# Performance work log

Hardware: AMD Instinct MI355X
Metric: run time of the kernel (lower is better)

The kernel has to match this reference:

```python
import jax, jax.numpy as jnp
import numpy as np

DIM = 1024
B = 8192
DT_REF_BASE = 1.0


def _cayley(raw_re, raw_im):
    # A = skew-Hermitian-ish combo per original code
    A = (raw_re - raw_re.T) * 0.5 + 1j * ((raw_im + raw_im.T) * 0.5)
    I = jnp.eye(A.shape[0], dtype=A.dtype)
    return jnp.linalg.solve(I - A, I + A)


def setup_inputs() -> dict:
    key = jax.random.key(0)
    ks = jax.random.split(key, 16)
    d = DIM
    g = d // 2  # n_groups = 2, equal group sizes
    return {
        "h_prev": jax.random.normal(ks[0], (B, d), jnp.float32),
        "x_input": jax.random.normal(ks[1], (B, d), jnp.float32),
        "dt": jax.random.uniform(ks[2], (B,), jnp.float32),
        "u_raw_re": jax.random.normal(ks[3], (d, d), jnp.float32) * 0.01,
        "u_raw_im": jax.random.normal(ks[4], (d, d), jnp.float32) * 0.01,
        "v_raw_re": jax.random.normal(ks[5], (d, d), jnp.float32) * 0.01,
        "v_raw_im": jax.random.normal(ks[6], (d, d), jnp.float32) * 0.01,
        "log_sigma": jnp.zeros((d,), jnp.float32),
        "ld": jax.random.normal(ks[7], (d,), jnp.float32) * 0.5 - 2.0,
        "lf": jnp.concatenate([
            2.0 * jax.random.normal(ks[8], (g,), jnp.float32),
            0.1 * jax.random.normal(ks[9], (g,), jnp.float32),
        ]),
        "dt_scaler": jnp.concatenate([0.1 * jnp.ones((g,), jnp.float32),
                                      10.0 * jnp.ones((g,), jnp.float32)]),
        "src_re": jax.random.normal(ks[10], (d,), jnp.float32) * 0.01,
        "src_im": jax.random.normal(ks[11], (d,), jnp.float32) * 0.01,
        "law_re": jax.random.normal(ks[12], (d,), jnp.float32) * 0.01,
        "law_im": jax.random.normal(ks[13], (d,), jnp.float32) * 0.01,
        "sel_w": jax.random.normal(ks[14], (2 * d, 2 * d), jnp.float32) * 0.01,
        "sel_b": jax.random.normal(ks[15], (2 * d,), jnp.float32) * 0.01,
    }


def reference(h_prev, x_input, dt, u_raw_re, u_raw_im, v_raw_re, v_raw_im,
              log_sigma, ld, lf, dt_scaler, src_re, src_im, law_re, law_im,
              sel_w, sel_b):
    # --- Cayley basis (shared between encode/decode) ---
    U = _cayley(u_raw_re, u_raw_im)                       # [D, D] complex
    V = _cayley(v_raw_re, v_raw_im)
    s = jnp.exp(log_sigma).astype(U.dtype)
    s_inv = jnp.exp(-log_sigma).astype(U.dtype)
    M_inv = (V * s_inv[None, :]) @ U.conj().T             # V @ diag(1/s) @ U^H
    M = (U * s[None, :]) @ V.conj().T                     # U @ diag(s) @ V^H

    encode = lambda x: x.astype(M_inv.dtype) @ M_inv.T
    h_tilde = encode(h_prev)[:, None, :]                  # [B, 1, D]
    x_tilde = encode(x_input)[:, None, :]                 # [B, 1, D]
    x_state = x_tilde[:, 0, :]                            # [B, D]

    # --- selective Lambda ---
    lam_static = (-jnp.exp(ld) + 1j * lf) + (law_re + 1j * law_im)  # [D]
    x_cat = jnp.concatenate([x_state.real, x_state.imag], axis=-1)  # [B, 2D]
    delta = x_cat @ sel_w.T + sel_b                                  # [B, 2D]
    d_re, d_im = jnp.split(delta, 2, axis=-1)
    Lam = lam_static[None, :] + (d_re + 1j * d_im)                   # [B, D]

    # --- transition operators ---
    dt_ref_eff = DT_REF_BASE * dt_scaler                  # [D]
    dt_n = dt[:, None] / dt_ref_eff                       # [B, D]
    Z = Lam * dt_n.astype(Lam.dtype)
    mask = jnp.abs(Z) < 1e-4
    safe_Z = jnp.where(mask, jnp.ones_like(Z), Z)
    phi1 = jnp.where(mask, 1.0 + 0.5 * Z + Z * Z / 6.0,
                     (jnp.exp(Z) - 1.0) / safe_Z)
    op_decay = jnp.exp(Z)                                 # [B, D]
    op_forcing = phi1 * (dt_n * dt_ref_eff).astype(Z.dtype)

    bias = src_re + 1j * src_im                           # [D]
    h_next = h_tilde * op_decay[:, None, :] + (x_tilde + bias) * op_forcing[:, None, :]
    # eval mode / noise term omitted (deterministic reference)
    return h_next @ M.T                                   # [B, 1, D] complex64
```

## Files before the change

### kernel.cpp

```cpp
#include <hip/hip_runtime.h>
#include <hip/hip_bf16.h>

#define Dd 1024
#define Bb 8192

typedef unsigned short u16;
typedef __attribute__((ext_vector_type(8))) short short8;
typedef __attribute__((ext_vector_type(4))) float f32x4;
typedef __attribute__((ext_vector_type(4))) float float4v;

static constexpr size_t DD  = (size_t)Dd * Dd;
static constexpr size_t BD  = (size_t)Bb * Dd;
static constexpr size_t MBy = 1ull << 20;

__device__ __forceinline__ float bf2f(u16 v) {
  union { unsigned u; float f; } c; c.u = ((unsigned)v) << 16; return c.f;
}
__device__ __forceinline__ u16 f2bf(float f) {
  union { float f; unsigned u; } c; c.f = f;
  return (u16)((c.u + 0x7fffu + ((c.u >> 16) & 1u)) >> 16);
}

union U64 { u16 u[4]; unsigned long long v; };

struct ZP { const u16* Ah; const u16* Al; const u16* Bh; const u16* Bl; void* C; void* C2; float alpha; float beta; };
struct GArgs { ZP z[8]; int K, lda, ldb; long ldc; int cstride; };

template<int OUT>
__device__ __forceinline__ void c_store(const ZP& p, long cidx, float acc) {
  float v = acc * p.alpha;
  if constexpr (OUT == 1) {
    ((u16*)p.C)[cidx] = f2bf(v);
  } else if constexpr (OUT == 2) {
    u16 h = f2bf(v);
    ((u16*)p.C)[cidx] = h;
    ((u16*)p.C2)[cidx] = f2bf(v - bf2f(h));
  } else {
    float* C = (float*)p.C;
    if (p.beta != 0.0f) v += p.beta * C[cidx];
    C[cidx] = v;
  }
}

template<int MODE, int OUT, int BN>
__global__ __launch_bounds__(256) void gemm_nt(GArgs a) {
  constexpr bool X2 = (MODE != 0);
  constexpr int BK  = X2 ? 32 : 64;
  constexpr int NJ  = BN / 32;
  constexpr int BUFS = 8192 + BN * 64;
  constexpr int BHOFF = 4096;
  constexpr int ALOFF = 4096 + BN * 32;
  constexpr int BLOFF = 8192 + BN * 32;
  __shared__ __align__(16) u16 smem[2 * BUFS];
  const ZP p = a.z[blockIdx.z];
  const int tid  = threadIdx.x;
  const int lane = tid & 63, wv = tid >> 6;

  int bx = blockIdx.x, by = blockIdx.y;
  {
    const int gx = gridDim.x;
    const int nwg = gx * gridDim.y;
    if ((nwg & 7) == 0 && nwg >= 16) {
      const int flat = by * gx + bx;
      const int ch = nwg >> 3;
      const int nf = (flat & 7) * ch + (flat >> 3);
      bx = nf % gx; by = nf / gx;
    }
  }

  const long brow = (long)by * 128, bcol = (long)bx * BN;
  const int wm = (wv & 1) * 64, wn = (wv >> 1) * (BN / 2);
  const int srow = wv * 8 + (lane >> 3);
  const int sgc64 = ((lane & 7) ^ (lane >> 3)) * 8;
  const int sgc32 = ((tid & 3) ^ ((tid >> 3) & 3)) * 8;

  f32x4 acc[4][NJ];
#pragma unroll
  for (int i = 0; i < 4; ++i)
#pragma unroll
    for (int j = 0; j < NJ; ++j) { f32x4 zv = {0.f, 0.f, 0.f, 0.f}; acc[i][j] = zv; }

  auto STAGE = [&](int kt, int buf) {
    u16* base = smem + buf * BUFS;
    if constexpr (!X2) {
      u16* As = base;
      u16* Bs = base + 8192;
#pragma unroll
      for (int i = 0; i < 4; ++i) {
        const int rr = i * 32 + srow;
        const int lb = (i * 32 + wv * 8) * 64;
        const u16* ga = p.Ah + (brow + rr) * (long)a.lda + kt + sgc64;
        __builtin_amdgcn_global_load_lds((const __attribute__((address_space(1))) void*)ga,
                                         (__attribute__((address_space(3))) void*)(As + lb), 16, 0, 0);
      }
#pragma unroll
      for (int i = 0; i < BN / 32; ++i) {
        const int rr = i * 32 + srow;
        const int lb = (i * 32 + wv * 8) * 64;
        const u16* gb = p.Bh + (bcol + rr) * (long)a.ldb + kt + sgc64;
        __builtin_amdgcn_global_load_lds((const __attribute__((address_space(1))) void*)gb,
                                         (__attribute__((address_space(3))) void*)(Bs + lb), 16, 0, 0);
      }
    } else {
#pragma unroll
      for (int pass = 0; pass < 2; ++pass) {
        const int row = pass * 64 + (tid >> 2);
        const int lb = pass * 2048 + tid * 8;
        const u16* ga = p.Ah + (brow + row) * (long)a.lda + kt + sgc32;
        const u16* ga2 = p.Al + (brow + row) * (long)a.lda + kt + sgc32;
        __builtin_amdgcn_global_load_lds((const __attribute__((address_space(1))) void*)ga,
                                         (__attribute__((address_space(3))) void*)(base + lb), 16, 0, 0);
        __builtin_amdgcn_global_load_lds((const __attribute__((address_space(1))) void*)ga2,
                                         (__attribute__((address_space(3))) void*)(base + ALOFF + lb), 16, 0, 0);
      }
#pragma unroll
      for (int pass = 0; pass < BN / 64; ++pass) {
        const int row = pass * 64 + (tid >> 2);
        const int lb = pass * 2048 + tid * 8;
        const u16* gb = p.Bh + (bcol + row) * (long)a.ldb + kt + sgc32;
        const u16* gb2 = p.Bl + (bcol + row) * (long)a.ldb + kt + sgc32;
        __builtin_amdgcn_global_load_lds((const __attribute__((address_space(1))) void*)gb,
                                         (__attribute__((address_space(3))) void*)(base + BHOFF + lb), 16, 0, 0);
        __builtin_amdgcn_global_load_lds((const __attribute__((address_space(1))) void*)gb2,
                                         (__attribute__((address_space(3))) void*)(base + BLOFF + lb), 16, 0, 0);
      }
    }
  };

  auto COMPUTE = [&](int buf) {
    u16* base = smem + buf * BUFS;
    if constexpr (!X2) {
      u16* As = base;
      u16* Bs = base + 8192;
#pragma unroll
      for (int kk = 0; kk < 64; kk += 32) {
        const int jf = (kk >> 3) + (lane >> 4);
        const int cs = ((jf ^ (lane & 7)) << 3);
        short8 af[4], bfv[NJ];
#pragma unroll
        for (int i = 0; i < 4; ++i)
          af[i] = *(const short8*)(As + (wm + i * 16 + (lane & 15)) * 64 + cs);
#pragma unroll
        for (int j = 0; j < NJ; ++j)
          bfv[j] = *(const short8*)(Bs + (wn + j * 16 + (lane & 15)) * 64 + cs);
#pragma unroll
        for (int i = 0; i < 4; ++i)
#pragma unroll
          for (int j = 0; j < NJ; ++j)
            acc[i][j] = __builtin_amdgcn_mfma_f32_16x16x32_bf16(af[i], bfv[j], acc[i][j], 0, 0, 0);
      }
    } else {
      const int jf = lane >> 4;
      const int cs = ((jf ^ ((lane >> 1) & 3)) << 3);
      short8 af[4], al[4], bfv[NJ], bl[NJ];
#pragma unroll
      for (int i = 0; i < 4; ++i) {
        const int ra = (wm + i * 16 + (lane & 15)) * 32 + cs;
        af[i] = *(const short8*)(base + ra);
        al[i] = *(const short8*)(base + ALOFF + ra);
      }
#pragma unroll
      for (int j = 0; j < NJ; ++j) {
        const int rb = (wn + j * 16 + (lane & 15)) * 32 + cs;
        bfv[j] = *(const short8*)(base + BHOFF + rb);
        bl[j]  = *(const short8*)(base + BLOFF + rb);
      }
#pragma unroll
      for (int i = 0; i < 4; ++i)
#pragma unroll
        for (int j = 0; j < NJ; ++j) {
          acc[i][j] = __builtin_amdgcn_mfma_f32_16x16x32_bf16(af[i], bfv[j], acc[i][j], 0, 0, 0);
          acc[i][j] = __builtin_amdgcn_mfma_f32_16x16x32_bf16(al[i], bfv[j], acc[i][j], 0, 0, 0);
          acc[i][j] = __builtin_amdgcn_mfma_f32_16x16x32_bf16(af[i], bl[j], acc[i][j], 0, 0, 0);
        }
    }
  };

  const int nkt = a.K / BK;
  STAGE(0, 0);
  __syncthreads();
  int cur = 0;
  for (int t = 0; t < nkt - 1; ++t) {
    STAGE((t + 1) * BK, cur ^ 1);
    COMPUTE(cur);
    __syncthreads();
    cur ^= 1;
  }
  COMPUTE(cur);

  const long crow = brow + wm + ((lane >> 4) * 4);
  const long ccol = bcol + wn + (lane & 15);
#pragma unroll
  for (int i = 0; i < 4; ++i)
#pragma unroll
    for (int j = 0; j < NJ; ++j)
#pragma unroll
      for (int r = 0; r < 4; ++r) {
        const long cidx = (crow + i * 16 + r) * a.ldc + (ccol + j * 16) * (long)a.cstride;
        c_store<OUT>(p, cidx, acc[i][j][r]);
      }
}

template<int OUT>
__global__ __launch_bounds__(512, 1) void gemm_nt256(GArgs a) {
  constexpr int BUFS = 32768;
  __shared__ __align__(16) u16 smem[2 * BUFS];
  const ZP p = a.z[blockIdx.z];
  const int tid  = threadIdx.x;
  const int lane = tid & 63, wv = tid >> 6;
  const int wr = wv >> 2, wc = wv & 3;

  int bx = blockIdx.x, by = blockIdx.y;
  {
    const int gx = gridDim.x;
    const int nwg = gx * gridDim.y;
    if ((nwg & 7) == 0 && nwg >= 16) {
      const int flat = by * gx + bx;
      const int ch = nwg >> 3;
      const int nf = (flat & 7) * ch + (flat >> 3);
      bx = nf % gx; by = nf / gx;
    }
  }

  const long brow = (long)by * 256, bcol = (long)bx * 256;
  const int sgc = ((tid & 7) ^ ((tid >> 3) & 7)) * 8;

  f32x4 acc[8][4];
#pragma unroll
  for (int i = 0; i < 8; ++i)
#pragma unroll
    for (int j = 0; j < 4; ++j) { f32x4 zv = {0.f, 0.f, 0.f, 0.f}; acc[i][j] = zv; }

  auto STAGE = [&](int kt, int buf) {
    u16* As = smem + buf * BUFS;
    u16* Bs = As + 16384;
#pragma unroll
    for (int i = 0; i < 4; ++i) {
      const int rr = i * 64 + (tid >> 3);
      const int lb = i * 4096 + tid * 8;
      const u16* ga = p.Ah + (brow + rr) * (long)a.lda + kt + sgc;
      const u16* gb = p.Bh + (bcol + rr) * (long)a.ldb + kt + sgc;
      __builtin_amdgcn_global_load_lds((const __attribute__((address_space(1))) void*)ga,
                                       (__attribute__((address_space(3))) void*)(As + lb), 16, 0, 0);
      __builtin_amdgcn_global_load_lds((const __attribute__((address_space(1))) void*)gb,
                                       (__attribute__((address_space(3))) void*)(Bs + lb), 16, 0, 0);
    }
  };

  auto COMPUTE = [&](int buf) {
    u16* As = smem + buf * BUFS;
    u16* Bs = As + 16384;
#pragma unroll
    for (int kk = 0; kk < 64; kk += 32) {
      const int jf = (kk >> 3) + (lane >> 4);
      const int cs = ((jf ^ (lane & 7)) << 3);
      short8 af[8], bfv[4];
#pragma unroll
      for (int i = 0; i < 8; ++i)
        af[i] = *(const short8*)(As + (wr * 128 + i * 16 + (lane & 15)) * 64 + cs);
#pragma unroll
      for (int j = 0; j < 4; ++j)
        bfv[j] = *(const short8*)(Bs + (wc * 64 + j * 16 + (lane & 15)) * 64 + cs);
#pragma unroll
      for (int i = 0; i < 8; ++i)
#pragma unroll
        for (int j = 0; j < 4; ++j)
          acc[i][j] = __builtin_amdgcn_mfma_f32_16x16x32_bf16(af[i], bfv[j], acc[i][j], 0, 0, 0);
    }
  };

  const int nkt = a.K >> 6;
  STAGE(0, 0);
  __syncthreads();
  int cur = 0;
  for (int t = 0; t < nkt - 1; ++t) {
    STAGE((t + 1) * 64, cur ^ 1);
    COMPUTE(cur);
    __syncthreads();
    cur ^= 1;
  }
  COMPUTE(cur);

  const long crow = brow + wr * 128 + ((lane >> 4) * 4);
  const long ccol = bcol + wc * 64 + (lane & 15);
#pragma unroll
  for (int i = 0; i < 8; ++i)
#pragma unroll
    for (int j = 0; j < 4; ++j)
#pragma unroll
      for (int r = 0; r < 4; ++r) {
        const long cidx = (crow + i * 16 + r) * a.ldc + (ccol + j * 16) * (long)a.cstride;
        c_store<OUT>(p, cidx, acc[i][j][r]);
      }
}

#define TLOAD(ldsbuf, srcp) do { \
  _Pragma("unroll") \
  for (int i_ = 0; i_ < 4; ++i_) { \
    int row_ = ty + i_ * 16; \
    float4v v_ = *(const float4v*)((srcp) + (size_t)row_ * Dd + tx * 4); \
    ldsbuf[row_][tx * 4 + 0] = v_[0]; ldsbuf[row_][tx * 4 + 1] = v_[1]; \
    ldsbuf[row_][tx * 4 + 2] = v_[2]; ldsbuf[row_][tx * 4 + 3] = v_[3]; \
  } } while (0)

__global__ void k_buildA(const float* ur, const float* ui, const float* vr, const float* vi,
                         float* Af32, u16* Ahi, u16* Alo, u16* AsumH, u16* AsumL) {
  __shared__ float ldsA[64][65], ldsB[64][65];
  const int y = blockIdx.z;
  const int tx = threadIdx.x & 15, ty = threadIdx.x >> 4;
  const int R0 = blockIdx.y * 64, C0 = blockIdx.x * 64;
  const float* re = y ? vr : ur; const float* im = y ? vi : ui;
  TLOAD(ldsA, re + (size_t)C0 * Dd + R0);
  TLOAD(ldsB, im + (size_t)C0 * Dd + R0);
  __syncthreads();
#pragma unroll
  for (int i = 0; i < 4; ++i) {
    const int r = R0 + ty + i * 16;
    const size_t base = (size_t)r * Dd + C0 + tx * 4;
    float4v vre = *(const float4v*)(re + base);
    float4v vim = *(const float4v*)(im + base);
    float4v oar, oai;
    U64 ph, pl, pih, pil, sh, sl;
#pragma unroll
    for (int j = 0; j < 4; ++j) {
      float are = 0.5f * (vre[j] - ldsA[tx * 4 + j][ty + i * 16]);
      float aim = 0.5f * (vim[j] + ldsB[tx * 4 + j][ty + i * 16]);
      oar[j] = are; oai[j] = aim;
      u16 h = f2bf(are); ph.u[j] = h; pl.u[j] = f2bf(are - bf2f(h));
      h = f2bf(aim); pih.u[j] = h; pil.u[j] = f2bf(aim - bf2f(h));
      float s = are + aim; h = f2bf(s); sh.u[j] = h; sl.u[j] = f2bf(s - bf2f(h));
    }
    const size_t pr = (size_t)y * 2 * DD + base, pi = pr + DD;
    *(float4v*)(Af32 + pr) = oar; *(float4v*)(Af32 + pi) = oai;
    *(unsigned long long*)(Ahi + pr) = ph.v; *(unsigned long long*)(Alo + pr) = pl.v;
    *(unsigned long long*)(Ahi + pi) = pih.v; *(unsigned long long*)(Alo + pi) = pil.v;
    const size_t ps = (size_t)y * DD + base;
    *(unsigned long long*)(AsumH + ps) = sh.v; *(unsigned long long*)(AsumL + ps) = sl.v;
  }
}

__global__ void k_sq(const float* T, float* A2u, float* A2v, u16* A2T, u16* A2Tsum) {
  __shared__ float ldsA[64][65], ldsB[64][65];
  const int y = blockIdx.z;
  const int tx = threadIdx.x & 15, ty = threadIdx.x >> 4;
  const int R0 = blockIdx.y * 64, C0 = blockIdx.x * 64;
  const float* t0p = T + (size_t)y * 3 * DD;
  const float* t2p = t0p + 2 * DD;
  TLOAD(ldsA, t2p + (size_t)C0 * Dd + R0);
  __syncthreads();
  float* A2 = y ? A2v : A2u;
  float xr[4][4], xi[4][4];
#pragma unroll
  for (int i = 0; i < 4; ++i) {
    const size_t base = (size_t)(R0 + ty + i * 16) * Dd + C0 + tx * 4;
    float4v v0 = *(const float4v*)(t0p + base);
    float4v v1 = *(const float4v*)(t0p + DD + base);
    float4v v2 = *(const float4v*)(t2p + base);
    float4v oar, oai;
#pragma unroll
    for (int j = 0; j < 4; ++j) {
      float a2re = -v0[j] - v1[j];
      float a2im = v2[j] - ldsA[tx * 4 + j][ty + i * 16];
      xr[i][j] = a2re; xi[i][j] = a2im;
      oar[j] = a2re; oai[j] = a2im;
    }
    *(float4v*)(A2 + base) = oar;
    *(float4v*)(A2 + DD + base) = oai;
  }
  __syncthreads();
#pragma unroll
  for (int i = 0; i < 4; ++i)
#pragma unroll
    for (int j = 0; j < 4; ++j) {
      ldsA[ty + i * 16][tx * 4 + j] = xr[i][j];
      ldsB[ty + i * 16][tx * 4 + j] = xi[i][j];
    }
  __syncthreads();
#pragma unroll
  for (int i = 0; i < 4; ++i) {
    const int cc = C0 + ty + i * 16;
    const size_t tb = (size_t)cc * Dd + R0 + tx * 4;
    U64 ph, pih, sh;
#pragma unroll
    for (int j = 0; j < 4; ++j) {
      float a2re = ldsA[tx * 4 + j][ty + i * 16];
      float a2im = ldsB[tx * 4 + j][ty + i * 16];
      ph.u[j] = f2bf(a2re); pih.u[j] = f2bf(a2im);
      sh.u[j] = f2bf(a2re + a2im);
    }
    const size_t qr = (size_t)y * 2 * DD + tb;
    *(unsigned long long*)(A2T + qr) = ph.v;
    *(unsigned long long*)(A2T + qr + DD) = pih.v;
    *(unsigned long long*)(A2Tsum + (size_t)y * DD + tb) = sh.v;
  }
}

__global__ void k_x0n(const float* Af32, const float* A2u, const float* A2v, const float* T,
                      float* Xf32, u16* Xhi, u16* XThi, u16* XsumH, u16* XTsumH) {
  __shared__ float ldsA[64][65], ldsB[64][65];
  const int y = blockIdx.z;
  const int tx = threadIdx.x & 15, ty = threadIdx.x >> 4;
  const int R0 = blockIdx.y * 64, C0 = blockIdx.x * 64;
  const float* t0p = T + (size_t)y * 3 * DD;
  const float* A2 = y ? A2v : A2u;
  float xr[4][4], xi[4][4];
#pragma unroll
  for (int i = 0; i < 4; ++i) {
    const int r = R0 + ty + i * 16;
    const size_t base = (size_t)r * Dd + C0 + tx * 4;
    float4v v0 = *(const float4v*)(t0p + base);
    float4v v1 = *(const float4v*)(t0p + DD + base);
    float4v v2 = *(const float4v*)(t0p + 2 * DD + base);
    const size_t pr = (size_t)y * 2 * DD + base, pi = pr + DD;
    float4v ar = *(const float4v*)(Af32 + pr);
    float4v ai = *(const float4v*)(Af32 + pi);
    float4v a2r = *(const float4v*)(A2 + base);
    float4v a2i = *(const float4v*)(A2 + DD + base);
    float4v oxr, oxi;
    U64 ph, pih, sh;
#pragma unroll
    for (int j = 0; j < 4; ++j) {
      const int c = C0 + tx * 4 + j;
      float xre = ar[j] + a2r[j] + (v0[j] - v1[j]) + (r == c ? 1.0f : 0.0f);
      float xim = ai[j] + a2i[j] + (v2[j] - v0[j] - v1[j]);
      xr[i][j] = xre; xi[i][j] = xim;
      oxr[j] = xre; oxi[j] = xim;
      ph.u[j] = f2bf(xre); pih.u[j] = f2bf(xim);
      sh.u[j] = f2bf(xre + xim);
    }
    *(float4v*)(Xf32 + pr) = oxr; *(float4v*)(Xf32 + pi) = oxi;
    *(unsigned long long*)(Xhi + pr) = ph.v; *(unsigned long long*)(Xhi + pi) = pih.v;
    *(unsigned long long*)(XsumH + (size_t)y * DD + base) = sh.v;
  }
  __syncthreads();
#pragma unroll
  for (int i = 0; i < 4; ++i)
#pragma unroll
    for (int j = 0; j < 4; ++j) {
      ldsA[ty + i * 16][tx * 4 + j] = xr[i][j];
      ldsB[ty + i * 16][tx * 4 + j] = xi[i][j];
    }
  __syncthreads();
#pragma unroll
  for (int i = 0; i < 4; ++i) {
    const int cc = C0 + ty + i * 16;
    const size_t tb = (size_t)cc * Dd + R0 + tx * 4;
    U64 ph, pih, sh;
#pragma unroll
    for (int j = 0; j < 4; ++j) {
      float xre = ldsA[tx * 4 + j][ty + i * 16];
      float xim = ldsB[tx * 4 + j][ty + i * 16];
      ph.u[j] = f2bf(xre); pih.u[j] = f2bf(xim);
      sh.u[j] = f2bf(xre + xim);
    }
    const size_t qr = (size_t)y * 2 * DD + tb;
    *(unsigned long long*)(XThi + qr) = ph.v;
    *(unsigned long long*)(XThi + qr + DD) = pih.v;
    *(unsigned long long*)(XTsumH + (size_t)y * DD + tb) = sh.v;
  }
}

__global__ void k_wt(const float* Xf32, const float* T, u16* WThi, u16* WTsumH, float idc) {
  __shared__ float lds[64][65];
  const int y = blockIdx.z;
  const int tx = threadIdx.x & 15, ty = threadIdx.x >> 4;
  const int N0 = blockIdx.y * 64, K0 = blockIdx.x * 64;
  const float* t1p = T + (size_t)y * 3 * DD;
  const float* xrp = Xf32 + (size_t)y * 2 * DD;
  float wre[4][4], wim[4][4];
#pragma unroll
  for (int i = 0; i < 4; ++i)
#pragma unroll
    for (int j = 0; j < 4; ++j) {
      wre[i][j] = ((N0 + ty + i * 16) == (K0 + tx * 4 + j)) ? idc : 0.0f;
      wim[i][j] = 0.0f;
    }
  const float* planes[5] = {t1p, t1p + DD, t1p + 2 * DD, xrp, xrp + DD};
#pragma unroll
  for (int p = 0; p < 5; ++p) {
    TLOAD(lds, planes[p] + (size_t)K0 * Dd + N0);
    __syncthreads();
#pragma unroll
    for (int i = 0; i < 4; ++i)
#pragma unroll
      for (int j = 0; j < 4; ++j) {
        float v = lds[tx * 4 + j][ty + i * 16];
        if (p == 0) { wre[i][j] += v; wim[i][j] -= v; }
        else if (p == 1) { wre[i][j] -= v; wim[i][j] -= v; }
        else if (p == 2) { wim[i][j] += v; }
        else if (p == 3) { wre[i][j] -= v; }
        else { wim[i][j] -= v; }
      }
    __syncthreads();
  }
#pragma unroll
  for (int i = 0; i < 4; ++i) {
    const size_t base = (size_t)(N0 + ty + i * 16) * Dd + K0 + tx * 4;
    U64 ph, pih, sh;
#pragma unroll
    for (int j = 0; j < 4; ++j) {
      ph.u[j] = f2bf(wre[i][j]); pih.u[j] = f2bf(wim[i][j]);
      sh.u[j] = f2bf(wre[i][j] + wim[i][j]);
    }
    const size_t pr = (size_t)y * 2 * DD + base;
    *(unsigned long long*)(WThi + pr) = ph.v;
    *(unsigned long long*)(WThi + pr + DD) = pih.v;
    *(unsigned long long*)(WTsumH + (size_t)y * DD + base) = sh.v;
  }
}

__global__ void k_xn(const float* T, float* Xf32, u16* Xhi, u16* XThi, u16* XsumH, u16* XTsumH,
                     u16* Xlo, u16* XTlo, u16* XTsumL) {
  __shared__ float ldsA[64][65], ldsB[64][65];
  const int y = blockIdx.z;
  const int tx = threadIdx.x & 15, ty = threadIdx.x >> 4;
  const int R0 = blockIdx.y * 64, C0 = blockIdx.x * 64;
  const float* t1p = T + (size_t)y * 3 * DD;
  float xr[4][4], xi[4][4];
#pragma unroll
  for (int i = 0; i < 4; ++i) {
    const size_t base = (size_t)(R0 + ty + i * 16) * Dd + C0 + tx * 4;
    float4v v1 = *(const float4v*)(t1p + base);
    float4v v2 = *(const float4v*)(t1p + DD + base);
    float4v v3 = *(const float4v*)(t1p + 2 * DD + base);
    float4v oxr, oxi;
    U64 ph, pih, sh, plr, pli;
#pragma unroll
    for (int j = 0; j < 4; ++j) {
      float xre = v1[j] - v2[j];
      float xim = v3[j] - v1[j] - v2[j];
      xr[i][j] = xre; xi[i][j] = xim;
      oxr[j] = xre; oxi[j] = xim;
      u16 hr = f2bf(xre), hi_ = f2bf(xim);
      ph.u[j] = hr; pih.u[j] = hi_;
      sh.u[j] = f2bf(xre + xim);
      plr.u[j] = f2bf(xre - bf2f(hr)); pli.u[j] = f2bf(xim - bf2f(hi_));
    }
    const size_t pr = (size_t)y * 2 * DD + base, pi = pr + DD;
    *(float4v*)(Xf32 + pr) = oxr; *(float4v*)(Xf32 + pi) = oxi;
    *(unsigned long long*)(Xhi + pr) = ph.v; *(unsigned long long*)(Xhi + pi) = pih.v;
    *(unsigned long long*)(XsumH + (size_t)y * DD + base) = sh.v;
    if (Xlo) {
      *(unsigned long long*)(Xlo + pr) = plr.v;
      *(unsigned long long*)(Xlo + pi) = pli.v;
    }
  }
  __syncthreads();
#pragma unroll
  for (int i = 0; i < 4; ++i)
#pragma unroll
    for (int j = 0; j < 4; ++j) {
      ldsA[ty + i * 16][tx * 4 + j] = xr[i][j];
      ldsB[ty + i * 16][tx * 4 + j] = xi[i][j];
    }
  __syncthreads();
#pragma unroll
  for (int i = 0; i < 4; ++i) {
    const int cc = C0 + ty + i * 16;
    const size_t tb = (size_t)cc * Dd + R0 + tx * 4;
    U64 ph, pih, sh, plr, pli, sl;
#pragma unroll
    for (int j = 0; j < 4; ++j) {
      float xre = ldsA[tx * 4 + j][ty + i * 16];
      float xim = ldsB[tx * 4 + j][ty + i * 16];
      u16 hr = f2bf(xre), hi_ = f2bf(xim);
      ph.u[j] = hr; pih.u[j] = hi_;
      float s = xre + xim; u16 hs = f2bf(s);
      sh.u[j] = hs;
      plr.u[j] = f2bf(xre - bf2f(hr)); pli.u[j] = f2bf(xim - bf2f(hi_));
      sl.u[j] = f2bf(s - bf2f(hs));
    }
    const size_t qr = (size_t)y * 2 * DD + tb;
    *(unsigned long long*)(XThi + qr) = ph.v;
    *(unsigned long long*)(XThi + qr + DD) = pih.v;
    *(unsigned long long*)(XTsumH + (size_t)y * DD + tb) = sh.v;
    if (Xlo) {
      *(unsigned long long*)(XTlo + qr) = plr.v;
      *(unsigned long long*)(XTlo + qr + DD) = pli.v;
      *(unsigned long long*)(XTsumL + (size_t)y * DD + tb) = sl.v;
    }
  }
}

__global__ void k_finalUV(const float* Xf32, const float* T, const float* logsig,
                          u16* VsHi, u16* VsLo, u16* UHi, u16* ULo, u16* UsHi, u16* VHi,
                          u16* UdifH, u16* UdifL, u16* UssumH, u16* VssumH, u16* VssumL, u16* VdifH) {
  const int y = blockIdx.y;
  const size_t idx = (size_t)blockIdx.x * 256 + threadIdx.x;
  const size_t r = idx >> 10, c = idx & 1023;
  const size_t t0 = (size_t)y * 3 * DD;
  float t1 = T[t0 + idx], t2 = T[t0 + DD + idx], t3 = T[t0 + 2 * DD + idx];
  const size_t pr = (size_t)y * 2 * DD + idx, pi = pr + DD;
  float cre = 2.0f * (Xf32[pr] + (t1 - t2)) - (r == c ? 1.0f : 0.0f);
  float cim = 2.0f * (Xf32[pi] + (t3 - t1 - t2));
  if (y == 0) {
    u16 h = f2bf(cre); UHi[idx] = h; ULo[idx] = f2bf(cre - bf2f(h));
    h = f2bf(cim); UHi[DD + idx] = h; ULo[DD + idx] = f2bf(cim - bf2f(h));
    float d = cre - cim; h = f2bf(d); UdifH[idx] = h; UdifL[idx] = f2bf(d - bf2f(h));
    float s = expf(logsig[c]);
    UsHi[idx] = f2bf(cre * s); UsHi[DD + idx] = f2bf(cim * s);
    UssumH[idx] = f2bf((cre + cim) * s);
  } else {
    VHi[idx] = f2bf(cre); VHi[DD + idx] = f2bf(cim);
    VdifH[idx] = f2bf(cre - cim);
    float si = expf(-logsig[c]);
    float a = cre * si, b = cim * si;
    u16 h = f2bf(a); VsHi[idx] = h; VsLo[idx] = f2bf(a - bf2f(h));
    h = f2bf(b); VsHi[DD + idx] = h; VsLo[DD + idx] = f2bf(b - bf2f(h));
    float ss = (cre + cim) * si; h = f2bf(ss); VssumH[idx] = h; VssumL[idx] = f2bf(ss - bf2f(h));
  }
}

__global__ void k_cmb_M(const float* T, u16* MiRe, u16* MiIm, u16* MiTcH, u16* MiTcL,
                        u16* Mcat) {
  __shared__ float ldsA[64][65], ldsB[64][65];
  const int tx = threadIdx.x & 15, ty = threadIdx.x >> 4;
  const int R0 = blockIdx.y * 64, C0 = blockIdx.x * 64;
#pragma unroll
  for (int i = 0; i < 4; ++i) {
    const size_t base = (size_t)(R0 + ty + i * 16) * Dd + C0 + tx * 4;
    const size_t r = R0 + ty + i * 16;
    float4v g1 = *(const float4v*)(T + base);
    float4v g2 = *(const float4v*)(T + DD + base);
    float4v g3 = *(const float4v*)(T + 2 * DD + base);
    float4v h1 = *(const float4v*)(T + 3 * DD + base);
    float4v h2 = *(const float4v*)(T + 4 * DD + base);
    float4v h3 = *(const float4v*)(T + 5 * DD + base);
    U64 pir, pii, pmr, pmi;
#pragma unroll
    for (int j = 0; j < 4; ++j) {
      float mire = g1[j] + g2[j];
      float miim = g3[j] - g1[j] + g2[j];
      float mre  = h1[j] + h2[j];
      float mim  = h3[j] - h1[j] + h2[j];
      pir.u[j] = f2bf(mire); pii.u[j] = f2bf(miim);
      pmr.u[j] = f2bf(mre);  pmi.u[j] = f2bf(mim);
      ldsA[ty + i * 16][tx * 4 + j] = mire;
      ldsB[ty + i * 16][tx * 4 + j] = miim;
    }
    *(unsigned long long*)(MiRe + base) = pir.v;
    *(unsigned long long*)(MiIm + base) = pii.v;
    const size_t mb = r * 2048 + C0 + tx * 4;
    *(unsigned long long*)(Mcat + mb) = pmr.v;
    *(unsigned long long*)(Mcat + mb + 1024) = pmi.v;
  }
  __syncthreads();
#pragma unroll
  for (int i = 0; i < 4; ++i) {
    const int cc = C0 + ty + i * 16;
    const size_t o = (size_t)cc * 2048 + R0 + tx * 4;
    U64 rh, rl, ih, il;
#pragma unroll
    for (int j = 0; j < 4; ++j) {
      float mire = ldsA[tx * 4 + j][ty + i * 16];
      float miim = ldsB[tx * 4 + j][ty + i * 16];
      u16 h = f2bf(mire); rh.u[j] = h; rl.u[j] = f2bf(mire - bf2f(h));
      h = f2bf(miim); ih.u[j] = h; il.u[j] = f2bf(miim - bf2f(h));
    }
    *(unsigned long long*)(MiTcH + o) = rh.v;
    *(unsigned long long*)(MiTcL + o) = rl.v;
    *(unsigned long long*)(MiTcH + o + 1024) = ih.v;
    *(unsigned long long*)(MiTcL + o + 1024) = il.v;
  }
}

__global__ void k_split4(const float* src, u16* hi, u16* lo) {
  const size_t i4 = (size_t)blockIdx.x * 256 + threadIdx.x;
  float4v v = ((const float4v*)src)[i4];
  U64 oh, ol;
#pragma unroll
  for (int j = 0; j < 4; ++j) {
    u16 h = f2bf(v[j]);
    oh.u[j] = h; ol.u[j] = f2bf(v[j] - bf2f(h));
  }
  ((unsigned long long*)hi)[i4] = oh.v;
  ((unsigned long long*)lo)[i4] = ol.v;
}

__global__ void k_splitB(const float* x, const float* hsrc, u16* xh, u16* xl, u16* hb) {
  const size_t i4 = (size_t)blockIdx.x * 256 + threadIdx.x;
  float4v xv = ((const float4v*)x)[i4];
  float4v hv = ((const float4v*)hsrc)[i4];
  U64 oh, ol, ob;
#pragma unroll
  for (int j = 0; j < 4; ++j) {
    u16 h = f2bf(xv[j]);
    oh.u[j] = h;
    ol.u[j] = f2bf(xv[j] - bf2f(h));
    ob.u[j] = f2bf(hv[j]);
  }
  ((unsigned long long*)xh)[i4] = oh.v;
  ((unsigned long long*)xl)[i4] = ol.v;
  ((unsigned long long*)hb)[i4] = ob.v;
}

__global__ void k_pointwise(const u16* HtCat, const u16* XtCat,
                            const float* delta, const float* dt, const float* ld, const float* lf,
                            const float* dts, const float* sre, const float* sim,
                            const float* lwre, const float* lwim, const float* selb,
                            u16* Hncat, float imSign) {
  const int b = blockIdx.x;
  const int c0 = threadIdx.x * 4;
  const size_t ro = (size_t)b * 2048 + c0;
  const float dtv = dt[b];
  float4v dre4 = *(const float4v*)(delta + ro);
  float4v dim4 = *(const float4v*)(delta + ro + 1024);
  float4v sbR = *(const float4v*)(selb + c0);
  float4v sbI = *(const float4v*)(selb + 1024 + c0);
  float4v ld4 = *(const float4v*)(ld + c0);
  float4v lf4 = *(const float4v*)(lf + c0);
  float4v dts4 = *(const float4v*)(dts + c0);
  float4v sre4 = *(const float4v*)(sre + c0);
  float4v sim4 = *(const float4v*)(sim + c0);
  float4v lwr4 = *(const float4v*)(lwre + c0);
  float4v lwi4 = *(const float4v*)(lwim + c0);
  U64 htR, htI, xtR, xtI;
  htR.v = *(const unsigned long long*)(HtCat + ro);
  htI.v = *(const unsigned long long*)(HtCat + ro + 1024);
  xtR.v = *(const unsigned long long*)(XtCat + ro);
  xtI.v = *(const unsigned long long*)(XtCat + ro + 1024);
  U64 oR, oI;
#pragma unroll
  for (int j = 0; j < 4; ++j) {
    float lamre = -expf(ld4[j]) + lwr4[j] + dre4[j] + sbR[j];
    float lamim = lf4[j] + lwi4[j] + dim4[j] + sbI[j];
    float dtn = dtv / dts4[j];
    float zre = lamre * dtn, zim = lamim * dtn;
    float r2 = zre * zre + zim * zim;
    float er = expf(zre); float sn, cs; __sincosf(zim, &sn, &cs);
    float dcre = er * cs, dcim = er * sn;
    float p1re, p1im;
    if (r2 < 1e-8f) {
      p1re = 1.0f + 0.5f * zre + (zre * zre - zim * zim) * (1.0f / 6.0f);
      p1im = 0.5f * zim + (zre * zim) * (1.0f / 3.0f);
    } else {
      float inv = 1.0f / r2;
      float nre = dcre - 1.0f, nim = dcim;
      p1re = (nre * zre + nim * zim) * inv;
      p1im = (nim * zre - nre * zim) * inv;
    }
    float fre = p1re * dtv, fim = p1im * dtv;
    float hre = bf2f(htR.u[j]), him = bf2f(htI.u[j]);
    float xre = bf2f(xtR.u[j]) + sre4[j], xim = bf2f(xtI.u[j]) + sim4[j];
    float ore = hre * dcre - him * dcim + xre * fre - xim * fim;
    float oim = hre * dcim + him * dcre + xre * fim + xim * fre;
    oR.u[j] = f2bf(ore); oI.u[j] = f2bf(imSign * oim);
  }
  *(unsigned long long*)(Hncat + ro) = oR.v;
  *(unsigned long long*)(Hncat + ro + 1024) = oI.v;
}

__global__ void k_fill(float* p, size_t n, float v) {
  const size_t idx = (size_t)blockIdx.x * 256 + threadIdx.x;
  if (idx < n) p[idx] = v;
}

static void launch_gemm(int mode, int out, int M, int N, int K, int lda, int ldb,
                        long ldc, int cstride, int nz, const ZP* z, hipStream_t s) {
  GArgs a; a.K = K; a.lda = lda; a.ldb = ldb; a.ldc = ldc; a.cstride = cstride;
  for (int i = 0; i < 8; ++i) a.z[i] = z[i < nz ? i : 0];
  dim3 g(N / 128, M / 128, nz), blk(256);
  if (mode == 1 && out == 0)      gemm_nt<1, 0, 128><<<g, blk, 0, s>>>(a);
  else if (mode == 1 && out == 2) gemm_nt<1, 2, 128><<<g, blk, 0, s>>>(a);
  else                            gemm_nt<0, 0, 128><<<g, blk, 0, s>>>(a);
}

static void launch_gemm256(int out, int M, int N, int K, int lda, int ldb,
                           long ldc, int cstride, int nz, const ZP* z, hipStream_t s) {
  GArgs a; a.K = K; a.lda = lda; a.ldb = ldb; a.ldc = ldc; a.cstride = cstride;
  for (int i = 0; i < 8; ++i) a.z[i] = z[i < nz ? i : 0];
  dim3 g(N / 256, M / 256, nz), blk(512);
  if (out == 1) gemm_nt256<1><<<g, blk, 0, s>>>(a);
  else          gemm_nt256<0><<<g, blk, 0, s>>>(a);
}

extern "C" void kernel_launch(void* const* d_in, const int* in_sizes, int n_in,
                              void* d_out, int out_size, void* d_ws, size_t ws_size,
                              hipStream_t stream) {
  const float* h_prev  = (const float*)d_in[0];
  const float* x_input = (const float*)d_in[1];
  const float* dt      = (const float*)d_in[2];
  const float* ur      = (const float*)d_in[3];
  const float* ui      = (const float*)d_in[4];
  const float* vr      = (const float*)d_in[5];
  const float* vi      = (const float*)d_in[6];
  const float* logsig  = (const float*)d_in[7];
  const float* ld      = (const float*)d_in[8];
  const float* lf      = (const float*)d_in[9];
  const float* dts     = (const float*)d_in[10];
  const float* sre     = (const float*)d_in[11];
  const float* sim     = (const float*)d_in[12];
  const float* lwre    = (const float*)d_in[13];
  const float* lwim    = (const float*)d_in[14];
  const float* sel_w   = (const float*)d_in[15];
  const float* sel_b   = (const float*)d_in[16];
  float* out = (float*)d_out;
  char* ws = (char*)d_ws;

  const bool realOnly = ((size_t)out_size == BD);
  const bool interleaved = ((size_t)out_size == 2 * BD);
  if ((!realOnly && !interleaved) || ws_size < 224 * MBy) {
    k_fill<<<dim3(((size_t)out_size + 255) / 256), dim3(256), 0, stream>>>(out, (size_t)out_size, 1e9f);
    return;
  }

  u16* MiRe_b = (u16*)(ws + 0 * MBy);
  u16* MiIm_b = (u16*)(ws + 2 * MBy);
  u16* Mcat   = (u16*)(ws + 4 * MBy);
  u16* G_hi   = (u16*)(ws + 8 * MBy);
  u16* G_lo   = (u16*)(ws + 12 * MBy);
  char* AR = ws + 16 * MBy;
  float* Af32   = (float*)(AR + 0);
  u16* Ahi      = (u16*)(AR + 16 * MBy);
  u16* Alo      = (u16*)(AR + 24 * MBy);
  u16* AsumH    = (u16*)(AR + 32 * MBy);
  u16* AsumL    = (u16*)(AR + 36 * MBy);
  float* Xf32   = (float*)(AR + 40 * MBy);
  u16* Xhi      = (u16*)(AR + 56 * MBy);
  u16* Xlo      = (u16*)(AR + 64 * MBy);
  u16* XThi     = (u16*)(AR + 72 * MBy);
  u16* XTlo     = (u16*)(AR + 80 * MBy);
  u16* XsumH    = (u16*)(AR + 88 * MBy);
  u16* XTsumH   = (u16*)(AR + 92 * MBy);
  u16* XTsumL   = (u16*)(AR + 96 * MBy);
  u16* WThi     = (u16*)(AR + 100 * MBy);
  u16* WTsumH   = (u16*)(AR + 108 * MBy);
  float* T      = (float*)(AR + 112 * MBy);
  u16* VsHi     = (u16*)(AR + 136 * MBy);
  u16* VsLo     = (u16*)(AR + 140 * MBy);
  u16* UHi      = (u16*)(AR + 144 * MBy);
  u16* ULo      = (u16*)(AR + 148 * MBy);
  u16* UsHi     = (u16*)(AR + 152 * MBy);
  u16* VHi      = (u16*)(AR + 156 * MBy);
  u16* UdifH    = (u16*)(AR + 160 * MBy);
  u16* UdifL    = (u16*)(AR + 162 * MBy);
  u16* UssumH   = (u16*)(AR + 164 * MBy);
  u16* VssumH   = (u16*)(AR + 166 * MBy);
  u16* VssumL   = (u16*)(AR + 168 * MBy);
  u16* VdifH    = (u16*)(AR + 170 * MBy);
  u16* MiTcH    = (u16*)(AR + 172 * MBy);
  u16* MiTcL    = (u16*)(AR + 176 * MBy);
  u16* W_hi     = (u16*)(AR + 180 * MBy);
  u16* W_lo     = (u16*)(AR + 188 * MBy);
  float* A2u    = (float*)(AR + 64 * MBy);
  float* A2v    = (float*)(AR + 80 * MBy);
  u16* A2T      = (u16*)(AR + 100 * MBy);
  u16* A2Tsum   = (u16*)(AR + 108 * MBy);
  u16* Hb     = (u16*)(AR + 0);
  u16* XbHi   = (u16*)(AR + 16 * MBy);
  u16* XbLo   = (u16*)(AR + 32 * MBy);
  u16* HtCat  = (u16*)(AR + 48 * MBy);
  u16* XtCat  = (u16*)(AR + 80 * MBy);
  float* delta= (float*)(AR + 112 * MBy);
  u16* Hncat  = (u16*)(AR + 176 * MBy);

  dim3 b256(256);
  const dim3 tdd(16, 16, 2);

  k_buildA<<<tdd, b256, 0, stream>>>(ur, ui, vr, vi, Af32, Ahi, Alo, AsumH, AsumL);

  {
    ZP z[6];
    for (int y = 0; y < 2; ++y) {
      const u16* are = Ahi + (size_t)y * 2 * DD; const u16* aim = are + DD;
      float* t = T + (size_t)y * 3 * DD;
      z[y*3+0] = {are, nullptr, are, nullptr, t,          nullptr, 1.f, 0.f};
      z[y*3+1] = {aim, nullptr, aim, nullptr, t + DD,     nullptr, 1.f, 0.f};
      z[y*3+2] = {are, nullptr, aim, nullptr, t + 2*DD,   nullptr, 1.f, 0.f};
    }
    launch_gemm(0, 0, 1024, 1024, 1024, 1024, 1024, 1024, 1, 6, z, stream);
  }
  k_sq<<<tdd, b256, 0, stream>>>(T, A2u, A2v, A2T, A2Tsum);
  {
    ZP z[6];
    for (int y = 0; y < 2; ++y) {
      const u16* are = Ahi + (size_t)y*2*DD; const u16* aim = are + DD;
      const u16* a2r = A2T + (size_t)y*2*DD; const u16* a2i = a2r + DD;
      float* t = T + (size_t)y*3*DD;
      z[y*3+0] = {are, nullptr, a2r, nullptr, t,        nullptr, 1.f, 0.f};
      z[y*3+1] = {aim, nullptr, a2i, nullptr, t + DD,   nullptr, 1.f, 0.f};
      z[y*3+2] = {AsumH + (size_t)y*DD, nullptr, A2Tsum + (size_t)y*DD, nullptr, t + 2*DD, nullptr, 1.f, 0.f};
    }
    launch_gemm(0, 0, 1024, 1024, 1024, 1024, 1024, 1024, 1, 6, z, stream);
  }
  k_x0n<<<tdd, b256, 0, stream>>>(Af32, A2u, A2v, T, Xf32, Xhi, XThi, XsumH, XTsumH);

  {
    ZP z[6];
    for (int y = 0; y < 2; ++y) {
      const u16* are = Ahi + (size_t)y*2*DD; const u16* aim = are + DD;
      const u16* xtr = XThi + (size_t)y*2*DD; const u16* xti = xtr + DD;
      float* t = T + (size_t)y*3*DD;
      z[y*3+0] = {are, nullptr, xtr, nullptr, t,        nullptr, 1.f, 0.f};
      z[y*3+1] = {aim, nullptr, xti, nullptr, t + DD,   nullptr, 1.f, 0.f};
      z[y*3+2] = {AsumH + (size_t)y*DD, nullptr, XTsumH + (size_t)y*DD, nullptr, t + 2*DD, nullptr, 1.f, 0.f};
    }
    launch_gemm(0, 0, 1024, 1024, 1024, 1024, 1024, 1024, 1, 6, z, stream);
  }
  k_wt<<<tdd, b256, 0, stream>>>(Xf32, T, WThi, WTsumH, 2.0f);
  {
    ZP z[6];
    for (int y = 0; y < 2; ++y) {
      const u16* xre = Xhi + (size_t)y*2*DD; const u16* xim = xre + DD;
      const u16* wtr = WThi + (size_t)y*2*DD; const u16* wti = wtr + DD;
      float* t = T + (size_t)y*3*DD;
      z[y*3+0] = {xre, nullptr, wtr, nullptr, t,        nullptr, 1.f, 0.f};
      z[y*3+1] = {xim, nullptr, wti, nullptr, t + DD,   nullptr, 1.f, 0.f};
      z[y*3+2] = {XsumH + (size_t)y*DD, nullptr, WTsumH + (size_t)y*DD, nullptr, t + 2*DD, nullptr, 1.f, 0.f};
    }
    launch_gemm(0, 0, 1024, 1024, 1024, 1024, 1024, 1024, 1, 6, z, stream);
  }
  k_xn<<<tdd, b256, 0, stream>>>(T, Xf32, Xhi, XThi, XsumH, XTsumH, Xlo, XTlo, XTsumL);

  {
    ZP z[6];
    for (int y = 0; y < 2; ++y) {
      const u16* areh = Ahi + (size_t)y*2*DD; const u16* aimh = areh + DD;
      const u16* arel = Alo + (size_t)y*2*DD; const u16* aiml = arel + DD;
      const u16* xtrh = XThi + (size_t)y*2*DD; const u16* xtih = xtrh + DD;
      const u16* xtrl = XTlo + (size_t)y*2*DD; const u16* xtil = xtrl + DD;
      float* t = T + (size_t)y*3*DD;
      z[y*3+0] = {areh, arel, xtrh, xtrl, t,        nullptr, 1.f, 0.f};
      z[y*3+1] = {aimh, aiml, xtih, xtil, t + DD,   nullptr, 1.f, 0.f};
      z[y*3+2] = {AsumH + (size_t)y*DD, AsumL + (size_t)y*DD,
                  XTsumH + (size_t)y*DD, XTsumL + (size_t)y*DD, t + 2*DD, nullptr, 1.f, 0.f};
    }
    launch_gemm(1, 0, 1024, 1024, 1024, 1024, 1024, 1024, 1, 6, z, stream);
  }
  k_wt<<<tdd, b256, 0, stream>>>(Xf32, T, WThi, WTsumH, 1.0f);
  {
    ZP z[6];
    for (int y = 0; y < 2; ++y) {
      const u16* xre = Xhi + (size_t)y*2*DD; const u16* xim = xre + DD;
      const u16* rtr = WThi + (size_t)y*2*DD; const u16* rti = rtr + DD;
      float* t = T + (size_t)y*3*DD;
      z[y*3+0] = {xre, nullptr, rtr, nullptr, t,        nullptr, 1.f, 0.f};
      z[y*3+1] = {xim, nullptr, rti, nullptr, t + DD,   nullptr, 1.f, 0.f};
      z[y*3+2] = {XsumH + (size_t)y*DD, nullptr, WTsumH + (size_t)y*DD, nullptr, t + 2*DD, nullptr, 1.f, 0.f};
    }
    launch_gemm(0, 0, 1024, 1024, 1024, 1024, 1024, 1024, 1, 6, z, stream);
  }
  k_finalUV<<<dim3(4096, 2), b256, 0, stream>>>(Xf32, T, logsig, VsHi, VsLo, UHi, ULo, UsHi, VHi,
                                                UdifH, UdifL, UssumH, VssumH, VssumL, VdifH);

  {
    ZP z[3] = {
      {VsHi,      VsLo,      UHi,      ULo,      T,        nullptr, 1.f, 0.f},
      {VsHi + DD, VsLo + DD, UHi + DD, ULo + DD, T + DD,   nullptr, 1.f, 0.f},
      {VssumH,    VssumL,    UdifH,    UdifL,    T + 2*DD, nullptr, 1.f, 0.f}};
    launch_gemm(1, 0, 1024, 1024, 1024, 1024, 1024, 1024, 1, 3, z, stream);
  }
  {
    ZP z[3] = {
      {UsHi,      nullptr, VHi,      nullptr, T + 3*DD, nullptr, 1.f, 0.f},
      {UsHi + DD, nullptr, VHi + DD, nullptr, T + 4*DD, nullptr, 1.f, 0.f},
      {UssumH,    nullptr, VdifH,    nullptr, T + 5*DD, nullptr, 1.f, 0.f}};
    launch_gemm(0, 0, 1024, 1024, 1024, 1024, 1024, 1024, 1, 3, z, stream);
  }
  k_cmb_M<<<dim3(16, 16), b256, 0, stream>>>(T, MiRe_b, MiIm_b, MiTcH, MiTcL, Mcat);

  k_split4<<<dim3(4096), b256, 0, stream>>>(sel_w, W_hi, W_lo);
  {
    ZP z1[1] = {{W_hi, W_lo, MiTcH, MiTcL, G_hi, G_lo, 1.f, 0.f}};
    launch_gemm(1, 2, 2048, 1024, 2048, 2048, 2048, 1024, 1, 1, z1, stream);
  }

  k_splitB<<<dim3(8192), b256, 0, stream>>>(x_input, h_prev, XbHi, XbLo, Hb);
  {
    ZP z[2] = {
      {Hb,   nullptr, MiRe_b, nullptr, HtCat, nullptr, 1.f, 0.f},
      {XbHi, nullptr, MiRe_b, nullptr, XtCat, nullptr, 1.f, 0.f}};
    launch_gemm256(1, 8192, 2048, 1024, 1024, 1024, 2048, 1, 2, z, stream);
  }
  {
    ZP z[2] = {
      {XbHi, XbLo, G_hi,                     G_lo,                     delta,        nullptr, 1.f, 0.f},
      {XbHi, XbLo, G_hi + 1024 * (size_t)Dd, G_lo + 1024 * (size_t)Dd, delta + 1024, nullptr, 1.f, 0.f}};
    launch_gemm(1, 0, 8192, 512, 1024, 1024, 1024, 2048, 1, 2, z, stream);
  }
  {
    ZP z[2] = {
      {XbHi, nullptr, G_hi + 512 * (size_t)Dd,  nullptr, delta + 512,  nullptr, 1.f, 0.f},
      {XbHi, nullptr, G_hi + 1536 * (size_t)Dd, nullptr, delta + 1536, nullptr, 1.f, 0.f}};
    launch_gemm256(0, 8192, 512, 1024, 1024, 1024, 2048, 1, 2, z, stream);
  }

  if (realOnly) {
    k_pointwise<<<dim3(8192), b256, 0, stream>>>(HtCat, XtCat, delta, dt, ld, lf, dts,
                                                 sre, sim, lwre, lwim, sel_b, Hncat, -1.0f);
    ZP z1[1] = {{Hncat, nullptr, Mcat, nullptr, out, nullptr, 1.f, 0.f}};
    launch_gemm256(0, 8192, 1024, 2048, 2048, 2048, 1024, 1, 1, z1, stream);
  } else {
    k_pointwise<<<dim3(8192), b256, 0, stream>>>(HtCat, XtCat, delta, dt, ld, lf, dts,
                                                 sre, sim, lwre, lwim, sel_b, Hncat, -1.0f);
    {
      ZP z1[1] = {{Hncat, nullptr, Mcat, nullptr, out, nullptr, 1.f, 0.f}};
      launch_gemm256(0, 8192, 1024, 2048, 2048, 2048, 2048, 2, 1, z1, stream);
    }
    {
      ZP z1[1] = {{Hncat, nullptr, Mcat + 1024, nullptr, out + 1, nullptr, 1.f, 0.f}};
      launch_gemm256(0, 8192, 1024, 1024, 2048, 2048, 2048, 2, 1, z1, stream);
    }
    {
      ZP z1[1] = {{Hncat + 1024, nullptr, Mcat, nullptr, out + 1, nullptr, -1.f, 1.f}};
      launch_gemm256(0, 8192, 1024, 1024, 2048, 2048, 2048, 2, 1, z1, stream);
    }
  }
}
```

Measured before the change: 642.0 us.

## Deepen gemm_nt256 pipeline to four half-K stages with vmcnt-based waits

Restructures the 256x256 GEMM main loop from a double-buffered 64-wide K tile into a four-slot ring of 32-wide K stages, prefetching three stages ahead. A raw s_waitcnt vmcnt plus a single barrier per stage replaces the full __syncthreads, so loads stay in flight while MFMAs issue. The LDS layout is changed to pack two rows per 64-element line with a new XOR swizzle, and s_setprio raises priority around the MFMA block. This aims to hide global-load latency better, at the cost of more barriers per K and fragile hand-coded wait counts that depend on exact load counts.

```diff
diff --git a/kernel.cpp b/kernel.cpp
--- a/kernel.cpp
+++ b/kernel.cpp
@@ -203,8 +203,7 @@
 
 template<int OUT>
 __global__ __launch_bounds__(512, 1) void gemm_nt256(GArgs a) {
-  constexpr int BUFS = 32768;
-  __shared__ __align__(16) u16 smem[2 * BUFS];
+  __shared__ __align__(16) u16 smem[4 * 16384];
   const ZP p = a.z[blockIdx.z];
   const int tid  = threadIdx.x;
   const int lane = tid & 63, wv = tid >> 6;
@@ -223,7 +222,10 @@
   }
 
   const long brow = (long)by * 256, bcol = (long)bx * 256;
-  const int sgc = ((tid & 7) ^ ((tid >> 3) & 7)) * 8;
+  const int rp_t = tid >> 3;
+  const int e_t  = (tid & 7) ^ (rp_t & 7);
+  const int grh  = (rp_t << 1) + (e_t >> 2);
+  const int gco  = (e_t & 3) * 8;
 
   f32x4 acc[8][4];
 #pragma unroll
@@ -231,55 +233,60 @@
 #pragma unroll
     for (int j = 0; j < 4; ++j) { f32x4 zv = {0.f, 0.f, 0.f, 0.f}; acc[i][j] = zv; }
 
-  auto STAGE = [&](int kt, int buf) {
-    u16* As = smem + buf * BUFS;
-    u16* Bs = As + 16384;
-#pragma unroll
-    for (int i = 0; i < 4; ++i) {
-      const int rr = i * 64 + (tid >> 3);
-      const int lb = i * 4096 + tid * 8;
-      const u16* ga = p.Ah + (brow + rr) * (long)a.lda + kt + sgc;
-      const u16* gb = p.Bh + (bcol + rr) * (long)a.ldb + kt + sgc;
+  auto STAGE = [&](int hs) {
+    u16* base = smem + (hs & 3) * 16384;
+    const int kcol = hs * 32 + gco;
+#pragma unroll
+    for (int r = 0; r < 2; ++r) {
+      const int lb = r * 4096 + tid * 8;
+      const u16* ga = p.Ah + (brow + r * 128 + grh) * (long)a.lda + kcol;
+      const u16* gb = p.Bh + (bcol + r * 128 + grh) * (long)a.ldb + kcol;
       __builtin_amdgcn_global_load_lds((const __attribute__((address_space(1))) void*)ga,
-                                       (__attribute__((address_space(3))) void*)(As + lb), 16, 0, 0);
+                                       (__attribute__((address_space(3))) void*)(base + lb), 16, 0, 0);
       __builtin_amdgcn_global_load_lds((const __attribute__((address_space(1))) void*)gb,
-                                       (__attribute__((address_space(3))) void*)(Bs + lb), 16, 0, 0);
+                                       (__attribute__((address_space(3))) void*)(base + 8192 + lb), 16, 0, 0);
     }
   };
 
-  auto COMPUTE = [&](int buf) {
-    u16* As = smem + buf * BUFS;
-    u16* Bs = As + 16384;
-#pragma unroll
-    for (int kk = 0; kk < 64; kk += 32) {
-      const int jf = (kk >> 3) + (lane >> 4);
-      const int cs = ((jf ^ (lane & 7)) << 3);
-      short8 af[8], bfv[4];
-#pragma unroll
-      for (int i = 0; i < 8; ++i)
-        af[i] = *(const short8*)(As + (wr * 128 + i * 16 + (lane & 15)) * 64 + cs);
+  auto COMPUTE = [&](int hs) {
+    u16* base = smem + (hs & 3) * 16384;
+    const int jf = lane >> 4;
+    short8 af[8], bfv[4];
+#pragma unroll
+    for (int i = 0; i < 8; ++i) {
+      const int R = wr * 128 + i * 16 + (lane & 15);
+      const int rp = R >> 1;
+      const int pp = (((R & 1) << 2) | jf) ^ (rp & 7);
+      af[i] = *(const short8*)(base + rp * 64 + pp * 8);
+    }
+#pragma unroll
+    for (int j = 0; j < 4; ++j) {
+      const int R = wc * 64 + j * 16 + (lane & 15);
+      const int rp = R >> 1;
+      const int pp = (((R & 1) << 2) | jf) ^ (rp & 7);
+      bfv[j] = *(const short8*)(base + 8192 + rp * 64 + pp * 8);
+    }
+    __builtin_amdgcn_s_setprio(1);
+#pragma unroll
+    for (int i = 0; i < 8; ++i)
 #pragma unroll
       for (int j = 0; j < 4; ++j)
-        bfv[j] = *(const short8*)(Bs + (wc * 64 + j * 16 + (lane & 15)) * 64 + cs);
-#pragma unroll
-      for (int i = 0; i < 8; ++i)
-#pragma unroll
-        for (int j = 0; j < 4; ++j)
-          acc[i][j] = __builtin_amdgcn_mfma_f32_16x16x32_bf16(af[i], bfv[j], acc[i][j], 0, 0, 0);
-    }
+        acc[i][j] = __builtin_amdgcn_mfma_f32_16x16x32_bf16(af[i], bfv[j], acc[i][j], 0, 0, 0);
+    __builtin_amdgcn_s_setprio(0);
   };
 
-  const int nkt = a.K >> 6;
-  STAGE(0, 0);
-  __syncthreads();
-  int cur = 0;
-  for (int t = 0; t < nkt - 1; ++t) {
-    STAGE((t + 1) * 64, cur ^ 1);
-    COMPUTE(cur);
-    __syncthreads();
-    cur ^= 1;
-  }
-  COMPUTE(cur);
+  const int nhs = a.K >> 5;
+  STAGE(0); STAGE(1); STAGE(2);
+  for (int s = 0; s < nhs; ++s) {
+    if (s + 2 <= nhs - 1)      { asm volatile("s_waitcnt vmcnt(8)" ::: "memory"); }
+    else if (s + 1 <= nhs - 1) { asm volatile("s_waitcnt vmcnt(4)" ::: "memory"); }
+    else                       { asm volatile("s_waitcnt vmcnt(0)" ::: "memory"); }
+    __builtin_amdgcn_sched_barrier(0);
+    __builtin_amdgcn_s_barrier();
+    if (s + 3 < nhs) STAGE(s + 3);
+    COMPUTE(s);
+  }
+  __builtin_amdgcn_s_barrier();
 
   const long crow = brow + wr * 128 + ((lane >> 4) * 4);
   const long ccol = bcol + wc * 64 + (lane & 15);
```

After: 652.6 us. Within noise of the previous version (+1.7%).
